# Optimization experiments

Measured on AMD Instinct MI355X. Metric: run time of the kernel, lower is better.

## Reference

```python
import jax, jax.numpy as jnp
import numpy as np

B, T, HID = 1, 256, 2048
H, D = 16, 128
KD = H * D
CONV = 4
MAX_CG = 30
LAMB_LB = 0.25
NORM_EPS = 1e-5


def setup_inputs() -> dict:
    key = jax.random.key(0)
    ks = jax.random.split(key, 10)
    s = 0.02
    init_lamb = float(np.log(np.exp(1.0 - LAMB_LB) - 1.0))  # softplus^-1(1 - lower_bound)
    return {
        "hidden_states": jax.random.normal(ks[0], (B, T, HID), jnp.float32),
        "Wq": jax.random.normal(ks[1], (HID, KD), jnp.float32) * s,
        "Wk": jax.random.normal(ks[2], (HID, KD), jnp.float32) * s,
        "Wv": jax.random.normal(ks[3], (HID, KD), jnp.float32) * s,
        "Wa": jax.random.normal(ks[4], (HID, H), jnp.float32) * s,
        "ba": jnp.full((H,), 2.0, jnp.float32),
        "Wb": jax.random.normal(ks[5], (HID, H), jnp.float32) * s,
        "bb": jnp.zeros((H,), jnp.float32),
        "conv_wq": jax.random.normal(ks[6], (KD, CONV), jnp.float32) * s,
        "conv_wk": jax.random.normal(ks[7], (KD, CONV), jnp.float32) * s,
        "lambda_params": jnp.full((KD,), init_lamb, jnp.float32),
        "o_norm_w": jnp.ones((D,), jnp.float32),
        "Wo": jax.random.normal(ks[8], (KD, HID), jnp.float32) * s,
    }


def short_conv_silu(x, w):
    # depthwise causal conv over time; x [b,t,c], w [c,k]
    k = w.shape[1]
    xp = jnp.pad(x, ((0, 0), (k - 1, 0), (0, 0)))
    t = x.shape[1]
    y = xp[:, 0:t, :] * w[:, 0]
    for i in range(1, k):
        y = y + xp[:, i:i + t, :] * w[:, i]
    return jax.nn.silu(y)


def l2norm(x):
    return x * jax.lax.rsqrt(jnp.sum(x * x, -1, keepdims=True) + 1e-6)


def rmsnorm(x, w):
    return x * jax.lax.rsqrt(jnp.mean(x * x, -1, keepdims=True) + NORM_EPS) * w


def cg_solve(A, b):
    # solve A x = b per (batch, head) with fixed CG iterations, x0 = 0
    matvec = lambda p: jnp.einsum('bhij,bhj->bhi', A, p)
    x0 = jnp.zeros_like(b)
    rs0 = jnp.sum(b * b, -1)

    def body(i, st):
        xc, r, p, rs = st
        Ap = matvec(p)
        alpha = rs / (jnp.sum(p * Ap, -1) + 1e-12)
        xc = xc + alpha[..., None] * p
        r = r - alpha[..., None] * Ap
        rs_n = jnp.sum(r * r, -1)
        p = r + (rs_n / (rs + 1e-12))[..., None] * p
        return xc, r, p, rs_n

    xf, _, _, _ = jax.lax.fori_loop(0, MAX_CG, body, (x0, b, b, rs0))
    return xf


def mesa_recurrence(q, k, v, g, beta, lamb_diag):
    # q,k,v [b,t,h,d]; g,beta [b,t,h]; lamb_diag [h,d,d]
    def step(carry, inp):
        h_kk, h_kv = carry
        qt, kt, vt, gt, bt = inp
        decay = jnp.exp(gt)[..., None, None]
        b_ = bt[..., None, None]
        h_kk = h_kk * decay + b_ * (kt[..., :, None] * kt[..., None, :])
        h_kv = h_kv * decay + b_ * (kt[..., :, None] * vt[..., None, :])
        A = h_kk + lamb_diag[None]
        q_star = cg_solve(A, qt)
        ot = jnp.einsum('bhk,bhkv->bhv', q_star, h_kv)
        return (h_kk, h_kv), ot

    init = (jnp.zeros((B, H, D, D), q.dtype), jnp.zeros((B, H, D, D), q.dtype))
    xs = (q.transpose(1, 0, 2, 3), k.transpose(1, 0, 2, 3), v.transpose(1, 0, 2, 3),
          g.transpose(1, 0, 2), beta.transpose(1, 0, 2))
    _, o = jax.lax.scan(step, init, xs)
    return o.transpose(1, 0, 2, 3)  # [b,t,h,d]


def reference(hidden_states, Wq, Wk, Wv, Wa, ba, Wb, bb, conv_wq, conv_wk,
              lambda_params, o_norm_w, Wo):
    x = hidden_states
    q = short_conv_silu(x @ Wq, conv_wq)
    k = short_conv_silu(x @ Wk, conv_wk)
    v = x @ Wv
    q = l2norm(q.reshape(B, T, H, D))
    k = l2norm(k.reshape(B, T, H, D))
    v = v.reshape(B, T, H, D)
    beta = jax.nn.sigmoid(x @ Wb + bb)          # [b,t,h]
    g = jax.nn.log_sigmoid(x @ Wa + ba)          # [b,t,h]
    lamb = (jax.nn.softplus(lambda_params) + LAMB_LB).reshape(H, D)
    lamb_diag = lamb[:, :, None] * jnp.eye(D, dtype=lamb.dtype)  # [h,d,d]
    o = mesa_recurrence(q, k, v, g, beta, lamb_diag)
    o = rmsnorm(o, o_norm_w)
    o = o.reshape(B, T, KD) @ Wo
    return o
```

## Files before the change

### kernel.cpp

```cpp
#include <hip/hip_runtime.h>
#include <math.h>

#define TT 256
#define HIDDEN 2048
#define NH 16
#define HD 128
#define KDIM 2048
#define NCG 30

typedef _Float16 h2 __attribute__((ext_vector_type(2)));
typedef _Float16 h4 __attribute__((ext_vector_type(4)));
typedef _Float16 half8 __attribute__((ext_vector_type(8)));
typedef float floatx4 __attribute__((ext_vector_type(4)));

__device__ __forceinline__ float wave_sum64(float v) {
#pragma unroll
    for (int off = 32; off > 0; off >>= 1) v += __shfl_xor(v, off, 64);
    return v;
}

__device__ __forceinline__ half8 cvt8(const float4 x, const float4 y) {
    half8 f;
    f[0] = (_Float16)x.x; f[1] = (_Float16)x.y; f[2] = (_Float16)x.z; f[3] = (_Float16)x.w;
    f[4] = (_Float16)y.x; f[5] = (_Float16)y.y; f[6] = (_Float16)y.z; f[7] = (_Float16)y.w;
    return f;
}

__device__ __forceinline__ void glds16(const void* g, void* l) {
    __builtin_amdgcn_global_load_lds(
        (const __attribute__((address_space(1))) void*)g,
        (__attribute__((address_space(3))) void*)l, 16, 0, 0);
}

__global__ __launch_bounds__(256) void wtrans_kernel(
    const float* __restrict__ W0, const float* __restrict__ W1,
    const float* __restrict__ W2, const float* __restrict__ W3,
    _Float16* __restrict__ T0, _Float16* __restrict__ T1,
    _Float16* __restrict__ T2, _Float16* __restrict__ T3,
    const float* __restrict__ Wa, const float* __restrict__ Wb,
    float* __restrict__ Tab)
{
    const int z = blockIdx.z;
    if (z == 4) {
        const int b = blockIdx.y * 32 + blockIdx.x;
        if (b < 256) {
            const int idx = b * 256 + threadIdx.x;
            const int k = idx & 2047;
            const int h = (idx >> 11) & 15;
            const int which = idx >> 15;
            const float* __restrict__ Wsrc = which ? Wb : Wa;
            Tab[(which * 16 + h) * KDIM + k] = Wsrc[k * NH + h];
        }
        return;
    }
    __shared__ float tile[64][68];
    const float* __restrict__ W = (z == 0) ? W0 : (z == 1) ? W1 : (z == 2) ? W2 : W3;
    _Float16* __restrict__ T = (z == 0) ? T0 : (z == 1) ? T1 : (z == 2) ? T2 : T3;
    const int k0 = blockIdx.x * 64, n0 = blockIdx.y * 64;
    const int tid = threadIdx.x;
#pragma unroll
    for (int p = 0; p < 4; p++) {
        const int idx = p * 256 + tid;
        const int r = idx >> 4, c = (idx & 15) * 4;
        const float4 v = *(const float4*)&W[(size_t)(k0 + r) * KDIM + n0 + c];
        tile[r][c] = v.x; tile[r][c + 1] = v.y; tile[r][c + 2] = v.z; tile[r][c + 3] = v.w;
    }
    __syncthreads();
#pragma unroll
    for (int p = 0; p < 2; p++) {
        const int slot = p * 256 + tid;
        const int ktc = slot >> 6, nn_loc = slot & 63;
        const int gk = k0 + ktc * 8, gn = n0 + nn_loc;
        const int nt = gn >> 7, nn = gn & 127;
        const int kt = gk >> 5, kc = (gk >> 3) & 3;
        half8 o;
#pragma unroll
        for (int j = 0; j < 8; j++) o[j] = (_Float16)tile[ktc * 8 + j][nn_loc];
        *(half8*)&T[(size_t)(((nt * 64 + kt) * 4 + kc)) * 1024 + nn * 8] = o;
    }
}

#define ASTR 72
__global__ __launch_bounds__(256) void gemm_kernel(
    const float* __restrict__ A,
    const _Float16* __restrict__ Bb0, const _Float16* __restrict__ Bb1,
    const _Float16* __restrict__ Bb2,
    float* __restrict__ C0, float* __restrict__ C1, float* __restrict__ C2,
    int nTilesPerMat)
{
    __shared__ __align__(16) _Float16 Bsh[2][8192];
    __shared__ __align__(16) _Float16 Ash[2][32 * ASTR];

    const int tid = threadIdx.x, lane = tid & 63, w = tid >> 6;
    const int q = lane >> 4, l16 = lane & 15;
    const int nt = blockIdx.x, mt = blockIdx.y;
    const int mat = nt / nTilesPerMat;
    const int ntile = nt - mat * nTilesPerMat;
    const int n0 = ntile * 128;
    const _Float16* __restrict__ Bb = (mat == 0) ? Bb0 : (mat == 1) ? Bb1 : Bb2;
    float* __restrict__ C = (mat == 0) ? C0 : (mat == 1) ? C1 : C2;
    const int m0 = mt * 32;

    const _Float16* __restrict__ Btile = Bb + (size_t)ntile * 262144;
    const int ar = tid >> 3, ac = (tid & 7) * 8;
    const float* __restrict__ Ap = &A[(size_t)(m0 + ar) * KDIM + ac];

    floatx4 acc[2][2] = {};
    float4 ax, ay;

#pragma unroll
    for (int i = 0; i < 4; i++)
        glds16(Btile + (size_t)((w * 4 + i) * 64 + lane) * 8, &Bsh[0][(w * 4 + i) * 512]);
    ax = *(const float4*)&Ap[0]; ay = *(const float4*)&Ap[4];
    *(half8*)&Ash[0][ar * ASTR + ac] = cvt8(ax, ay);
    ax = *(const float4*)&Ap[64]; ay = *(const float4*)&Ap[68];
    __syncthreads();

    const int NSTEP = KDIM / 64;
    for (int s = 0; s < NSTEP; s++) {
        const int cur = s & 1;
        if (s + 1 < NSTEP) {
            const _Float16* src = Btile + (size_t)(s + 1) * 8192;
#pragma unroll
            for (int i = 0; i < 4; i++)
                glds16(src + (size_t)((w * 4 + i) * 64 + lane) * 8, &Bsh[cur ^ 1][(w * 4 + i) * 512]);
        }
#pragma unroll
        for (int kk = 0; kk < 2; kk++) {
            const half8 bf0 = *(const half8*)&Bsh[cur][kk * 4096 + q * 1024 + (w * 32 + l16) * 8];
            const half8 bf1 = *(const half8*)&Bsh[cur][kk * 4096 + q * 1024 + (w * 32 + 16 + l16) * 8];
            const half8 af0 = *(const half8*)&Ash[cur][l16 * ASTR + kk * 32 + q * 8];
            const half8 af1 = *(const half8*)&Ash[cur][(16 + l16) * ASTR + kk * 32 + q * 8];
            acc[0][0] = __builtin_amdgcn_mfma_f32_16x16x32_f16(af0, bf0, acc[0][0], 0, 0, 0);
            acc[0][1] = __builtin_amdgcn_mfma_f32_16x16x32_f16(af0, bf1, acc[0][1], 0, 0, 0);
            acc[1][0] = __builtin_amdgcn_mfma_f32_16x16x32_f16(af1, bf0, acc[1][0], 0, 0, 0);
            acc[1][1] = __builtin_amdgcn_mfma_f32_16x16x32_f16(af1, bf1, acc[1][1], 0, 0, 0);
        }
        if (s + 1 < NSTEP) {
            *(half8*)&Ash[cur ^ 1][ar * ASTR + ac] = cvt8(ax, ay);
            if (s + 2 < NSTEP) {
                ax = *(const float4*)&Ap[(s + 2) * 64];
                ay = *(const float4*)&Ap[(s + 2) * 64 + 4];
            }
        }
        __syncthreads();
    }

#pragma unroll
    for (int r = 0; r < 4; r++) {
        C[(size_t)(m0 + q * 4 + r) * KDIM + n0 + w * 32 + l16] = acc[0][0][r];
        C[(size_t)(m0 + q * 4 + r) * KDIM + n0 + w * 32 + 16 + l16] = acc[0][1][r];
        C[(size_t)(m0 + 16 + q * 4 + r) * KDIM + n0 + w * 32 + l16] = acc[1][0][r];
        C[(size_t)(m0 + 16 + q * 4 + r) * KDIM + n0 + w * 32 + 16 + l16] = acc[1][1][r];
    }
}

__global__ __launch_bounds__(256) void ab_kernel(
    const float* __restrict__ X, const float* __restrict__ Tab,
    const float* __restrict__ ba, const float* __restrict__ bb,
    float* __restrict__ g, float* __restrict__ beta)
{
    const int t = blockIdx.x;
    const int lane = threadIdx.x & 63, w = threadIdx.x >> 6;
    for (int oi = 0; oi < 8; oi++) {
        const int o = w * 8 + oi;
        const int h = o & 15, which = o >> 4;
        float acc = 0.f;
#pragma unroll
        for (int i = 0; i < 8; i++) {
            const int kk = lane * 4 + i * 256;
            const float4 xv = *(const float4*)&X[t * HIDDEN + kk];
            const float4 wv = *(const float4*)&Tab[o * KDIM + kk];
            acc = fmaf(xv.x, wv.x, acc); acc = fmaf(xv.y, wv.y, acc);
            acc = fmaf(xv.z, wv.z, acc); acc = fmaf(xv.w, wv.w, acc);
        }
        acc = wave_sum64(acc);
        if (lane == 0) {
            if (which == 0) {
                const float z = acc + ba[h];
                g[t * NH + h] = fminf(z, 0.f) - log1pf(__expf(-fabsf(z)));
            } else {
                const float z = acc + bb[h];
                beta[t * NH + h] = 1.f / (1.f + __expf(-z));
            }
        }
    }
}

__global__ __launch_bounds__(256) void conv_silu_l2_kernel(
    const float* __restrict__ q_pre, const float* __restrict__ k_pre,
    const float* __restrict__ cwq, const float* __restrict__ cwk,
    float* __restrict__ qn, float* __restrict__ kn)
{
    const int t = blockIdx.x, h = blockIdx.y;
    const int which = threadIdx.x >> 7, d = threadIdx.x & 127;
    const int w = threadIdx.x >> 6;
    const int c = h * HD + d;
    const float* pre = which ? k_pre : q_pre;
    const float* cw  = which ? cwk : cwq;
    float y = 0.f;
#pragma unroll
    for (int i = 0; i < 4; i++) {
        const int ts = t - 3 + i;
        if (ts >= 0) y = fmaf(pre[ts * KDIM + c], cw[c * 4 + i], y);
    }
    const float s = y / (1.f + __expf(-y));
    float v = s * s;
#pragma unroll
    for (int off = 32; off > 0; off >>= 1) v += __shfl_down(v, off, 64);
    __shared__ float red[4];
    if ((threadIdx.x & 63) == 0) red[w] = v;
    __syncthreads();
    const float sum = red[which * 2] + red[which * 2 + 1];
    float* dst = which ? kn : qn;
    dst[t * KDIM + c] = s * rsqrtf(sum + 1e-6f);
}

#define PSTR 136
#define YSTR 264

template<int SMAX>
__device__ __forceinline__ void mesa_cg(
    const float* __restrict__ qn, const float* __restrict__ kn, const float* __restrict__ vv,
    const float* __restrict__ g, const float* __restrict__ bet, const float* __restrict__ lp,
    const float* __restrict__ onw, float* __restrict__ out,
    int h, int t0, _Float16* Psh, _Float16* Ysh, float* red,
    float* Gsh, float* bets)
{
    constexpr int NSUB1 = SMAX / 64;
    constexpr int NK2   = SMAX / 32;

    const int tid = threadIdx.x, lane = tid & 63, w = tid >> 6;
    const int quad = lane >> 4, l16 = lane & 15;
    const int tmy = t0 + l16;
    const int dbase = w * 32;

    {
        float sc = g[tid * NH + h];
#pragma unroll
        for (int off = 1; off < 64; off <<= 1) {
            const float o = __shfl_up(sc, off, 64);
            if (lane >= off) sc += o;
        }
        if (lane == 63) red[w] = sc;
        bets[tid] = bet[tid * NH + h];
        __syncthreads();
        float woff = 0.f;
        for (int u = 0; u < w; u++) woff += red[u];
        Gsh[tid] = sc + woff;
        __syncthreads();
    }

    half8 K1[NSUB1][4];
#pragma unroll
    for (int ii = 0; ii < NSUB1; ii++) {
        const int srow = 16 * (w + 4 * ii) + l16;
        const float* kp = &kn[(srow * NH + h) * HD];
#pragma unroll
        for (int kk = 0; kk < 4; kk++) {
            const float4 a = *(const float4*)&kp[kk * 32 + quad * 8];
            const float4 b = *(const float4*)&kp[kk * 32 + quad * 8 + 4];
            K1[ii][kk] = cvt8(a, b);
        }
    }

    half8 KtF[2][NK2];
#pragma unroll
    for (int ss = 0; ss < 2; ss++) {
        const int d = dbase + ss * 16 + l16;
#pragma unroll
        for (int kk = 0; kk < NK2; kk++) {
#pragma unroll
            for (int j = 0; j < 8; j++) {
                const int s = kk * 32 + quad * 8 + j;
                KtF[ss][kk][j] = (_Float16)kn[(s * NH + h) * HD + d];
            }
        }
    }

    half8 Vf[NK2][2];
#pragma unroll
    for (int kk = 0; kk < NK2; kk++) {
#pragma unroll
        for (int ss = 0; ss < 2; ss++) {
            const int dv = dbase + ss * 16 + l16;
#pragma unroll
            for (int j = 0; j < 8; j++) {
                const int s = kk * 32 + quad * 8 + j;
                Vf[kk][ss][j] = (_Float16)vv[(s * NH + h) * HD + dv];
            }
        }
    }

    const float Gt = Gsh[tmy];
    float Wm[NSUB1][4];
#pragma unroll
    for (int ii = 0; ii < NSUB1; ii++)
#pragma unroll
        for (int r = 0; r < 4; r++) {
            const int s = 16 * (w + 4 * ii) + quad * 4 + r;
            Wm[ii][r] = (s <= tmy) ? bets[s] * __expf(Gt - Gsh[s]) : 0.f;
        }
    float lam[8], xv[8], rv[8], pv[8];
#pragma unroll
    for (int ss = 0; ss < 2; ss++)
#pragma unroll
        for (int r = 0; r < 4; r++) {
            const int e = ss * 4 + r;
            const int d = dbase + ss * 16 + quad * 4 + r;
            const float lx = lp[h * HD + d];
            lam[e] = fmaxf(lx, 0.f) + log1pf(__expf(-fabsf(lx))) + 0.25f;
            const float b = qn[(tmy * NH + h) * HD + d];
            xv[e] = 0.f; rv[e] = b; pv[e] = b;
        }
    float rs = 0.f;
#pragma unroll
    for (int e = 0; e < 8; e++) rs += rv[e] * rv[e];
    rs += __shfl_xor(rs, 16, 64); rs += __shfl_xor(rs, 32, 64);

    auto writeP = [&](const float* src) {
#pragma unroll
        for (int ss = 0; ss < 2; ss++) {
            h4 ph;
            ph.x = (_Float16)src[ss * 4 + 0]; ph.y = (_Float16)src[ss * 4 + 1];
            ph.z = (_Float16)src[ss * 4 + 2]; ph.w = (_Float16)src[ss * 4 + 3];
            *(h4*)&Psh[l16 * PSTR + dbase + ss * 16 + quad * 4] = ph;
        }
    };
    writeP(pv);

    for (int it = 0; it <= NCG; it++) {
        __syncthreads();
        floatx4 acc1a[NSUB1] = {}, acc1b[NSUB1] = {};
#pragma unroll
        for (int kk = 0; kk < 2; kk++) {
            const half8 bfa = *(const half8*)&Psh[l16 * PSTR + kk * 32 + quad * 8];
            const half8 bfb = *(const half8*)&Psh[l16 * PSTR + (kk + 2) * 32 + quad * 8];
#pragma unroll
            for (int ii = 0; ii < NSUB1; ii++) {
                acc1a[ii] = __builtin_amdgcn_mfma_f32_16x16x32_f16(K1[ii][kk], bfa, acc1a[ii], 0, 0, 0);
                acc1b[ii] = __builtin_amdgcn_mfma_f32_16x16x32_f16(K1[ii][kk + 2], bfb, acc1b[ii], 0, 0, 0);
            }
        }
#pragma unroll
        for (int ii = 0; ii < NSUB1; ii++) {
            h4 yh;
            yh.x = (_Float16)(Wm[ii][0] * (acc1a[ii][0] + acc1b[ii][0]));
            yh.y = (_Float16)(Wm[ii][1] * (acc1a[ii][1] + acc1b[ii][1]));
            yh.z = (_Float16)(Wm[ii][2] * (acc1a[ii][2] + acc1b[ii][2]));
            yh.w = (_Float16)(Wm[ii][3] * (acc1a[ii][3] + acc1b[ii][3]));
            *(h4*)&Ysh[l16 * YSTR + 16 * (w + 4 * ii) + quad * 4] = yh;
        }
        __syncthreads();
        if (it == NCG) break;

        floatx4 acc2a[2] = {}, acc2b[2] = {};
#pragma unroll
        for (int kk = 0; kk < NK2; kk += 2) {
            const half8 bf0 = *(const half8*)&Ysh[l16 * YSTR + kk * 32 + quad * 8];
            const half8 bf1 = *(const half8*)&Ysh[l16 * YSTR + (kk + 1) * 32 + quad * 8];
#pragma unroll
            for (int ss = 0; ss < 2; ss++) {
                acc2a[ss] = __builtin_amdgcn_mfma_f32_16x16x32_f16(KtF[ss][kk], bf0, acc2a[ss], 0, 0, 0);
                acc2b[ss] = __builtin_amdgcn_mfma_f32_16x16x32_f16(KtF[ss][kk + 1], bf1, acc2b[ss], 0, 0, 0);
            }
        }
        float Ap[8], pAp = 0.f;
#pragma unroll
        for (int ss = 0; ss < 2; ss++)
#pragma unroll
            for (int r = 0; r < 4; r++) {
                const int e = ss * 4 + r;
                Ap[e] = (acc2a[ss][r] + acc2b[ss][r]) + lam[e] * pv[e];
                pAp = fmaf(pv[e], Ap[e], pAp);
            }
        pAp += __shfl_xor(pAp, 16, 64); pAp += __shfl_xor(pAp, 32, 64);
        const float alpha = rs / (pAp + 1e-12f);
        float rsn = 0.f;
#pragma unroll
        for (int e = 0; e < 8; e++) {
            xv[e] = fmaf(alpha, pv[e], xv[e]);
            rv[e] = fmaf(-alpha, Ap[e], rv[e]);
            rsn = fmaf(rv[e], rv[e], rsn);
        }
        rsn += __shfl_xor(rsn, 16, 64); rsn += __shfl_xor(rsn, 32, 64);
        const float bcg = rsn / (rs + 1e-12f);
#pragma unroll
        for (int e = 0; e < 8; e++) pv[e] = fmaf(bcg, pv[e], rv[e]);
        rs = rsn;
        writeP(it == NCG - 1 ? xv : pv);
    }

    floatx4 accOa[2] = {}, accOb[2] = {};
#pragma unroll
    for (int kk = 0; kk < NK2; kk += 2) {
        const half8 af0 = *(const half8*)&Ysh[l16 * YSTR + kk * 32 + quad * 8];
        const half8 af1 = *(const half8*)&Ysh[l16 * YSTR + (kk + 1) * 32 + quad * 8];
#pragma unroll
        for (int ss = 0; ss < 2; ss++) {
            accOa[ss] = __builtin_amdgcn_mfma_f32_16x16x32_f16(af0, Vf[kk][ss], accOa[ss], 0, 0, 0);
            accOb[ss] = __builtin_amdgcn_mfma_f32_16x16x32_f16(af1, Vf[kk + 1][ss], accOb[ss], 0, 0, 0);
        }
    }
    float accO[2][4];
#pragma unroll
    for (int ss = 0; ss < 2; ss++)
#pragma unroll
        for (int r = 0; r < 4; r++) accO[ss][r] = accOa[ss][r] + accOb[ss][r];

    float part[4];
#pragma unroll
    for (int r = 0; r < 4; r++) {
        part[r] = accO[0][r] * accO[0][r] + accO[1][r] * accO[1][r];
#pragma unroll
        for (int off = 1; off < 16; off <<= 1) part[r] += __shfl_xor(part[r], off, 64);
    }
    if (l16 == 0) {
#pragma unroll
        for (int r = 0; r < 4; r++) red[w * 16 + quad * 4 + r] = part[r];
    }
    __syncthreads();
    const float w0 = onw[dbase + l16], w1 = onw[dbase + 16 + l16];
#pragma unroll
    for (int r = 0; r < 4; r++) {
        const int qr = quad * 4 + r;
        const float sumd = red[qr] + red[16 + qr] + red[32 + qr] + red[48 + qr];
        const float sc = rsqrtf(sumd * (1.f / HD) + 1e-5f);
        const int trow = ((t0 + qr) * NH + h) * HD;
        out[trow + dbase + l16] = accO[0][r] * sc * w0;
        out[trow + dbase + 16 + l16] = accO[1][r] * sc * w1;
    }
}

__global__ __launch_bounds__(256, 1) void mesa_kernel(
    const float* __restrict__ qn, const float* __restrict__ kn, const float* __restrict__ vv,
    const float* __restrict__ g, const float* __restrict__ bet, const float* __restrict__ lp,
    const float* __restrict__ onw, float* __restrict__ out)
{
    __shared__ __align__(16) _Float16 Psh[16 * PSTR];
    __shared__ __align__(16) _Float16 Ysh[16 * YSTR];
    __shared__ float red[64];
    __shared__ float Gsh[256];
    __shared__ float bets[256];
    const int h = blockIdx.x, jb = blockIdx.y, t0 = jb * 16;
    switch (jb >> 2) {
        case 0:  mesa_cg<64> (qn, kn, vv, g, bet, lp, onw, out, h, t0, Psh, Ysh, red, Gsh, bets); break;
        case 1:  mesa_cg<128>(qn, kn, vv, g, bet, lp, onw, out, h, t0, Psh, Ysh, red, Gsh, bets); break;
        case 2:  mesa_cg<192>(qn, kn, vv, g, bet, lp, onw, out, h, t0, Psh, Ysh, red, Gsh, bets); break;
        default: mesa_cg<256>(qn, kn, vv, g, bet, lp, onw, out, h, t0, Psh, Ysh, red, Gsh, bets); break;
    }
}

extern "C" void kernel_launch(void* const* d_in, const int* in_sizes, int n_in,
                              void* d_out, int out_size, void* d_ws, size_t ws_size,
                              hipStream_t stream)
{
    (void)in_sizes; (void)n_in; (void)out_size; (void)ws_size;
    const float* x   = (const float*)d_in[0];
    const float* Wq  = (const float*)d_in[1];
    const float* Wk  = (const float*)d_in[2];
    const float* Wv  = (const float*)d_in[3];
    const float* Wa  = (const float*)d_in[4];
    const float* ba  = (const float*)d_in[5];
    const float* Wb  = (const float*)d_in[6];
    const float* bb  = (const float*)d_in[7];
    const float* cwq = (const float*)d_in[8];
    const float* cwk = (const float*)d_in[9];
    const float* lp  = (const float*)d_in[10];
    const float* onw = (const float*)d_in[11];
    const float* Wo  = (const float*)d_in[12];

    char* wsb = (char*)d_ws;
    float* q_pre = (float*)wsb;
    float* k_pre = q_pre + 524288;
    float* v     = k_pre + 524288;
    float* qn    = v + 524288;
    float* kn    = qn + 524288;
    float* g     = kn + 524288;
    float* beta  = g + 4096;
    float* G     = beta + 4096;
    float* lamb  = G + 4096;
    size_t off = ((size_t)((char*)(lamb + 2048) - wsb) + 1023) & ~(size_t)1023;
    _Float16* WtQ = (_Float16*)(wsb + off);
    _Float16* WtK = WtQ + (size_t)KDIM * KDIM;
    _Float16* WtV = WtK + (size_t)KDIM * KDIM;
    _Float16* WtO = WtV + (size_t)KDIM * KDIM;
    float* Tab    = (float*)(WtO + (size_t)KDIM * KDIM);
    float* onorm  = q_pre;
    float* outp   = (float*)d_out;

    wtrans_kernel<<<dim3(32, 32, 5), 256, 0, stream>>>(Wq, Wk, Wv, Wo, WtQ, WtK, WtV, WtO,
                                                       Wa, Wb, Tab);

    gemm_kernel<<<dim3(48, 8), 256, 0, stream>>>(x, WtQ, WtK, WtV, q_pre, k_pre, v, 16);
    ab_kernel<<<dim3(TT), 256, 0, stream>>>(x, Tab, ba, bb, g, beta);
    conv_silu_l2_kernel<<<dim3(TT, NH), 256, 0, stream>>>(q_pre, k_pre, cwq, cwk, qn, kn);

    mesa_kernel<<<dim3(NH, 16), 256, 0, stream>>>(qn, kn, v, g, beta, lp, onw, onorm);

    gemm_kernel<<<dim3(16, 8), 256, 0, stream>>>(onorm, WtO, WtO, WtO, outp, outp, outp, 16);
}
```

Before: 236.4 us.

## Fold gate projections into QKV GEMM, add XCD-aware tiling and 64-wide output GEMM

The separate ab_kernel is removed. The Wa/Wb projections are transposed to fp16 into an extra 128-column tile, which the main GEMM handles as a 49th N-tile, with the log-sigmoid and sigmoid epilogue applied in place. Block indices are remapped so that each XCD gets a contiguous set of N-tiles, which should improve L2 reuse of weights. The output projection gets a 64-column GEMM variant with 256 blocks instead of 128, to fill more CUs. The trade-off is that the gate projections now run in fp16 instead of fp32, and most of the extra gate tile is padded zero work.

After: 226.9 us. 4.0% less time.

```diff
diff --git a/kernel.cpp b/kernel.cpp
--- a/kernel.cpp
+++ b/kernel.cpp
@@ -38,32 +38,42 @@
     _Float16* __restrict__ T0, _Float16* __restrict__ T1,
     _Float16* __restrict__ T2, _Float16* __restrict__ T3,
     const float* __restrict__ Wa, const float* __restrict__ Wb,
-    float* __restrict__ Tab)
-{
+    _Float16* __restrict__ Tabb)
+{
+    __shared__ float tile[64][68];
     const int z = blockIdx.z;
+    const int tid = threadIdx.x;
+    int k0, n0;
+    _Float16* __restrict__ T;
+
     if (z == 4) {
-        const int b = blockIdx.y * 32 + blockIdx.x;
-        if (b < 256) {
-            const int idx = b * 256 + threadIdx.x;
-            const int k = idx & 2047;
-            const int h = (idx >> 11) & 15;
-            const int which = idx >> 15;
-            const float* __restrict__ Wsrc = which ? Wb : Wa;
-            Tab[(which * 16 + h) * KDIM + k] = Wsrc[k * NH + h];
-        }
-        return;
-    }
-    __shared__ float tile[64][68];
-    const float* __restrict__ W = (z == 0) ? W0 : (z == 1) ? W1 : (z == 2) ? W2 : W3;
-    _Float16* __restrict__ T = (z == 0) ? T0 : (z == 1) ? T1 : (z == 2) ? T2 : T3;
-    const int k0 = blockIdx.x * 64, n0 = blockIdx.y * 64;
-    const int tid = threadIdx.x;
-#pragma unroll
-    for (int p = 0; p < 4; p++) {
-        const int idx = p * 256 + tid;
-        const int r = idx >> 4, c = (idx & 15) * 4;
-        const float4 v = *(const float4*)&W[(size_t)(k0 + r) * KDIM + n0 + c];
-        tile[r][c] = v.x; tile[r][c + 1] = v.y; tile[r][c + 2] = v.z; tile[r][c + 3] = v.w;
+        const int y = blockIdx.y;
+        if (y >= 2) return;
+        k0 = blockIdx.x * 64; n0 = y * 64;
+        T = Tabb;
+#pragma unroll
+        for (int p = 0; p < 4; p++) {
+            const int idx = p * 256 + tid;
+            const int r = idx >> 4, c = (idx & 15) * 4;
+            float4 v = make_float4(0.f, 0.f, 0.f, 0.f);
+            if (y == 0 && c < 32) {
+                const float* src = (c < 16) ? &Wa[(size_t)(k0 + r) * NH + c]
+                                            : &Wb[(size_t)(k0 + r) * NH + (c - 16)];
+                v = *(const float4*)src;
+            }
+            tile[r][c] = v.x; tile[r][c + 1] = v.y; tile[r][c + 2] = v.z; tile[r][c + 3] = v.w;
+        }
+    } else {
+        const float* __restrict__ W = (z == 0) ? W0 : (z == 1) ? W1 : (z == 2) ? W2 : W3;
+        T = (z == 0) ? T0 : (z == 1) ? T1 : (z == 2) ? T2 : T3;
+        k0 = blockIdx.x * 64; n0 = blockIdx.y * 64;
+#pragma unroll
+        for (int p = 0; p < 4; p++) {
+            const int idx = p * 256 + tid;
+            const int r = idx >> 4, c = (idx & 15) * 4;
+            const float4 v = *(const float4*)&W[(size_t)(k0 + r) * KDIM + n0 + c];
+            tile[r][c] = v.x; tile[r][c + 1] = v.y; tile[r][c + 2] = v.z; tile[r][c + 3] = v.w;
+        }
     }
     __syncthreads();
 #pragma unroll
@@ -84,20 +94,26 @@
 __global__ __launch_bounds__(256) void gemm_kernel(
     const float* __restrict__ A,
     const _Float16* __restrict__ Bb0, const _Float16* __restrict__ Bb1,
-    const _Float16* __restrict__ Bb2,
+    const _Float16* __restrict__ Bb2, const _Float16* __restrict__ Bb3,
     float* __restrict__ C0, float* __restrict__ C1, float* __restrict__ C2,
-    int nTilesPerMat)
+    const float* __restrict__ ba, const float* __restrict__ bb,
+    float* __restrict__ g, float* __restrict__ beta)
 {
     __shared__ __align__(16) _Float16 Bsh[2][8192];
     __shared__ __align__(16) _Float16 Ash[2][32 * ASTR];
 
     const int tid = threadIdx.x, lane = tid & 63, w = tid >> 6;
     const int q = lane >> 4, l16 = lane & 15;
-    const int nt = blockIdx.x, mt = blockIdx.y;
-    const int mat = nt / nTilesPerMat;
-    const int ntile = nt - mat * nTilesPerMat;
+
+    const int b = blockIdx.x;
+    const int xcd = b & 7, gslot = b >> 3;
+    int nt, mt;
+    if (gslot < 48) { nt = xcd * 6 + (gslot >> 3); mt = gslot & 7; }
+    else           { nt = 48;                      mt = xcd; }
+    const int mat = nt >> 4;
+    const int ntile = nt & 15;
     const int n0 = ntile * 128;
-    const _Float16* __restrict__ Bb = (mat == 0) ? Bb0 : (mat == 1) ? Bb1 : Bb2;
+    const _Float16* __restrict__ Bb = (mat == 0) ? Bb0 : (mat == 1) ? Bb1 : (mat == 2) ? Bb2 : Bb3;
     float* __restrict__ C = (mat == 0) ? C0 : (mat == 1) ? C1 : C2;
     const int m0 = mt * 32;
 
@@ -146,6 +162,25 @@
         __syncthreads();
     }
 
+    if (mat == 3) {
+        if (w == 0) {
+            const float bav = ba[l16], bbv = bb[l16];
+#pragma unroll
+            for (int r = 0; r < 4; r++) {
+                const int t0r = m0 + q * 4 + r, t1r = m0 + 16 + q * 4 + r;
+                float z0 = acc[0][0][r] + bav;
+                g[t0r * NH + l16] = fminf(z0, 0.f) - log1pf(__expf(-fabsf(z0)));
+                float z1 = acc[0][1][r] + bbv;
+                beta[t0r * NH + l16] = 1.f / (1.f + __expf(-z1));
+                float z2 = acc[1][0][r] + bav;
+                g[t1r * NH + l16] = fminf(z2, 0.f) - log1pf(__expf(-fabsf(z2)));
+                float z3 = acc[1][1][r] + bbv;
+                beta[t1r * NH + l16] = 1.f / (1.f + __expf(-z3));
+            }
+        }
+        return;
+    }
+
 #pragma unroll
     for (int r = 0; r < 4; r++) {
         C[(size_t)(m0 + q * 4 + r) * KDIM + n0 + w * 32 + l16] = acc[0][0][r];
@@ -155,35 +190,71 @@
     }
 }
 
-__global__ __launch_bounds__(256) void ab_kernel(
-    const float* __restrict__ X, const float* __restrict__ Tab,
-    const float* __restrict__ ba, const float* __restrict__ bb,
-    float* __restrict__ g, float* __restrict__ beta)
-{
-    const int t = blockIdx.x;
-    const int lane = threadIdx.x & 63, w = threadIdx.x >> 6;
-    for (int oi = 0; oi < 8; oi++) {
-        const int o = w * 8 + oi;
-        const int h = o & 15, which = o >> 4;
-        float acc = 0.f;
-#pragma unroll
-        for (int i = 0; i < 8; i++) {
-            const int kk = lane * 4 + i * 256;
-            const float4 xv = *(const float4*)&X[t * HIDDEN + kk];
-            const float4 wv = *(const float4*)&Tab[o * KDIM + kk];
-            acc = fmaf(xv.x, wv.x, acc); acc = fmaf(xv.y, wv.y, acc);
-            acc = fmaf(xv.z, wv.z, acc); acc = fmaf(xv.w, wv.w, acc);
-        }
-        acc = wave_sum64(acc);
-        if (lane == 0) {
-            if (which == 0) {
-                const float z = acc + ba[h];
-                g[t * NH + h] = fminf(z, 0.f) - log1pf(__expf(-fabsf(z)));
-            } else {
-                const float z = acc + bb[h];
-                beta[t * NH + h] = 1.f / (1.f + __expf(-z));
-            }
-        }
+__global__ __launch_bounds__(256) void gemm64_kernel(
+    const float* __restrict__ A, const _Float16* __restrict__ Bb,
+    float* __restrict__ C)
+{
+    __shared__ __align__(16) _Float16 Bsh[2][4096];
+    __shared__ __align__(16) _Float16 Ash[2][32 * ASTR];
+
+    const int tid = threadIdx.x, lane = tid & 63, w = tid >> 6;
+    const int q = lane >> 4, l16 = lane & 15;
+    const int b = blockIdx.x;
+    const int xcd = b & 7, gslot = b >> 3;
+    const int nt = xcd * 4 + (gslot >> 3), mt = gslot & 7;
+    const int n0 = nt * 64, m0 = mt * 32;
+    const int nt128 = nt >> 1;
+    const size_t nnoff = (size_t)(nt & 1) * 512;
+
+    const _Float16* __restrict__ Btile = Bb + (size_t)nt128 * 262144;
+    const int ar = tid >> 3, ac = (tid & 7) * 8;
+    const float* __restrict__ Ap = &A[(size_t)(m0 + ar) * KDIM + ac];
+
+    floatx4 acc0 = {}, acc1 = {};
+    float4 ax, ay;
+
+    const int c0 = w * 2, c1 = w * 2 + 1;
+    auto bsrc = [&](int s, int chunk) {
+        const int kt2 = chunk >> 2, kc = chunk & 3;
+        return Btile + (size_t)((s * 2 + kt2) * 4 + kc) * 1024 + nnoff + (size_t)lane * 8;
+    };
+
+    glds16(bsrc(0, c0), &Bsh[0][c0 * 512]);
+    glds16(bsrc(0, c1), &Bsh[0][c1 * 512]);
+    ax = *(const float4*)&Ap[0]; ay = *(const float4*)&Ap[4];
+    *(half8*)&Ash[0][ar * ASTR + ac] = cvt8(ax, ay);
+    ax = *(const float4*)&Ap[64]; ay = *(const float4*)&Ap[68];
+    __syncthreads();
+
+    const int NSTEP = KDIM / 64;
+    for (int s = 0; s < NSTEP; s++) {
+        const int cur = s & 1;
+        if (s + 1 < NSTEP) {
+            glds16(bsrc(s + 1, c0), &Bsh[cur ^ 1][c0 * 512]);
+            glds16(bsrc(s + 1, c1), &Bsh[cur ^ 1][c1 * 512]);
+        }
+#pragma unroll
+        for (int kk = 0; kk < 2; kk++) {
+            const half8 bf  = *(const half8*)&Bsh[cur][kk * 2048 + q * 512 + (w * 16 + l16) * 8];
+            const half8 af0 = *(const half8*)&Ash[cur][l16 * ASTR + kk * 32 + q * 8];
+            const half8 af1 = *(const half8*)&Ash[cur][(16 + l16) * ASTR + kk * 32 + q * 8];
+            acc0 = __builtin_amdgcn_mfma_f32_16x16x32_f16(af0, bf, acc0, 0, 0, 0);
+            acc1 = __builtin_amdgcn_mfma_f32_16x16x32_f16(af1, bf, acc1, 0, 0, 0);
+        }
+        if (s + 1 < NSTEP) {
+            *(half8*)&Ash[cur ^ 1][ar * ASTR + ac] = cvt8(ax, ay);
+            if (s + 2 < NSTEP) {
+                ax = *(const float4*)&Ap[(s + 2) * 64];
+                ay = *(const float4*)&Ap[(s + 2) * 64 + 4];
+            }
+        }
+        __syncthreads();
+    }
+
+#pragma unroll
+    for (int r = 0; r < 4; r++) {
+        C[(size_t)(m0 + q * 4 + r) * KDIM + n0 + w * 16 + l16] = acc0[r];
+        C[(size_t)(m0 + 16 + q * 4 + r) * KDIM + n0 + w * 16 + l16] = acc1[r];
     }
 }
 
@@ -485,18 +556,18 @@
     _Float16* WtK = WtQ + (size_t)KDIM * KDIM;
     _Float16* WtV = WtK + (size_t)KDIM * KDIM;
     _Float16* WtO = WtV + (size_t)KDIM * KDIM;
-    float* Tab    = (float*)(WtO + (size_t)KDIM * KDIM);
+    _Float16* Tabb = WtO + (size_t)KDIM * KDIM;
     float* onorm  = q_pre;
     float* outp   = (float*)d_out;
 
     wtrans_kernel<<<dim3(32, 32, 5), 256, 0, stream>>>(Wq, Wk, Wv, Wo, WtQ, WtK, WtV, WtO,
-                                                       Wa, Wb, Tab);
-
-    gemm_kernel<<<dim3(48, 8), 256, 0, stream>>>(x, WtQ, WtK, WtV, q_pre, k_pre, v, 16);
-    ab_kernel<<<dim3(TT), 256, 0, stream>>>(x, Tab, ba, bb, g, beta);
+                                                       Wa, Wb, Tabb);
+
+    gemm_kernel<<<dim3(392), 256, 0, stream>>>(x, WtQ, WtK, WtV, Tabb,
+                                               q_pre, k_pre, v, ba, bb, g, beta);
     conv_silu_l2_kernel<<<dim3(TT, NH), 256, 0, stream>>>(q_pre, k_pre, cwq, cwk, qn, kn);
 
     mesa_kernel<<<dim3(NH, 16), 256, 0, stream>>>(qn, kn, v, g, beta, lp, onw, onorm);
 
-    gemm_kernel<<<dim3(16, 8), 256, 0, stream>>>(onorm, WtO, WtO, WtO, outp, outp, outp, 16);
-}
+    gemm64_kernel<<<dim3(256), 256, 0, stream>>>(onorm, WtO, outp);
+}
```
